# Performance work log

Hardware: AMD Instinct MI355X
Metric: run time of the kernel (lower is better)

The kernel has to match this reference:

```python
import jax, jax.numpy as jnp
import numpy as np

HIDDEN = 128
POOL = 64
G = 4            # grid_size
NBHD = 2.0       # neighborhood_size (meters)
NUM_SCENES = 256
PEDS = 64        # pedestrians per scene (uniform seq_start_end)


def setup_inputs() -> dict:
    key = jax.random.key(0)
    k1, k2, k3 = jax.random.split(key, 3)
    hidden_states = jax.random.normal(k1, (NUM_SCENES * PEDS, HIDDEN), jnp.float32)
    positions = jax.random.uniform(k2, (NUM_SCENES * PEDS, 2), jnp.float32)
    fan_in = HIDDEN * G * G
    weight = jax.random.normal(k3, (fan_in, POOL), jnp.float32) / np.sqrt(fan_in)
    bias = jnp.zeros((POOL,), jnp.float32)
    return {
        "hidden_states": hidden_states,
        "positions": positions,
        "weight": weight,
        "bias": bias,
        "peds_per_scene": PEDS,
    }


def reference(hidden_states, positions, weight, bias, peds_per_scene):
    total, H = hidden_states.shape
    P = peds_per_scene
    B = total // P
    h = hidden_states.reshape(B, P, H)
    p = positions.reshape(B, P, 2)

    # rel[b, i, j] = pos[j] - pos[i]  (matches curr_pos - curr_pos[i:i+1])
    rel = p[:, None, :, :] - p[:, :, None, :]            # [B, P, P, 2]
    in_range = (jnp.abs(rel[..., 0]) <= NBHD) & (jnp.abs(rel[..., 1]) <= NBHD)
    not_self = ~jnp.eye(P, dtype=bool)[None]
    mask = in_range & not_self                            # [B, P, P]

    # int() truncation == floor here since (rel + NBHD) >= 0 inside the range check
    scale = G / (2.0 * NBHD)
    gx = jnp.clip(jnp.floor((rel[..., 0] + NBHD) * scale).astype(jnp.int32), 0, G - 1)
    gy = jnp.clip(jnp.floor((rel[..., 1] + NBHD) * scale).astype(jnp.int32), 0, G - 1)
    grid_idx = gy * G + gx                                # [B, P, P]

    # scatter-add of neighbor hidden states into G*G bins via masked one-hot
    onehot = jax.nn.one_hot(grid_idx, G * G, dtype=h.dtype) * mask[..., None].astype(h.dtype)
    grid = jnp.einsum('bijg,bjh->bigh', onehot, h)        # [B, P, G*G, H]

    flat = grid.reshape(B * P, G * G * H)                 # row-major: (grid_idx, hidden)
    return flat @ weight + bias                            # [total_peds, POOL]
```

## Files before the change

kernel.cpp:

```cpp
#include <hip/hip_runtime.h>
#include <cstdint>

#define PEDS   64
#define HIDDEN 128
#define POOL   64
#define GRIDG  4
#define NBHD   2.0f

typedef unsigned short u16;
typedef unsigned int   u32;
typedef __attribute__((ext_vector_type(8))) short bf16x8;
typedef __attribute__((ext_vector_type(4))) float f32x4;

__device__ __forceinline__ u16 f2bf(float f) {
    u32 u = __float_as_uint(f);
    u += 0x7fffu + ((u >> 16) & 1u);
    return (u16)(u >> 16);
}
__device__ __forceinline__ u32 pack2bf(float a, float b) {
    return (u32)f2bf(a) | ((u32)f2bf(b) << 16);
}

__global__ __launch_bounds__(256, 2) void social_onepass(
    const float* __restrict__ h, const float* __restrict__ pos,
    const float* __restrict__ w, const float* __restrict__ bias,
    float* __restrict__ out)
{
    const int tid  = threadIdx.x;
    const int mt   = tid >> 6;
    const int lane = tid & 63;
    const int l15  = lane & 15;
    const int q    = lane >> 4;
    const int scene = blockIdx.x >> 1;
    const int ch    = blockIdx.x & 1;

    float2 pp = ((const float2*)pos)[(size_t)scene * PEDS + lane];

    const int i = mt * 16 + l15;
    const float pxi = __shfl(pp.x, i), pyi = __shfl(pp.y, i);
    const float scale = (float)GRIDG / (2.0f * NBHD);
    u32 gpk[4] = {0u, 0u, 0u, 0u};
    u32 um = 0u;
#pragma unroll
    for (int kk = 0; kk < 2; ++kk) {
#pragma unroll
        for (int e = 0; e < 8; ++e) {
            int j = kk * 32 + q * 8 + e;
            float rx = __shfl(pp.x, j) - pxi;
            float ry = __shfl(pp.y, j) - pyi;
            u32 gb = 0xffu;
            if ((i != j) && (fabsf(rx) <= NBHD) && (fabsf(ry) <= NBHD)) {
                int gx = (int)floorf((rx + NBHD) * scale); gx = min(max(gx, 0), GRIDG - 1);
                int gy = (int)floorf((ry + NBHD) * scale); gy = min(max(gy, 0), GRIDG - 1);
                gb = (u32)(gy * GRIDG + gx);
                um |= 1u << gb;
            }
            gpk[kk * 2 + (e >> 2)] |= gb << ((e & 3) * 8);
        }
    }
#pragma unroll
    for (int off = 32; off; off >>= 1) um |= __shfl_xor(um, off);
    um = __builtin_amdgcn_readfirstlane(um);

    const float* hbase = h + (size_t)scene * (PEDS * HIDDEN);
    const int jrow = (l15 >> 2) * 8 + (l15 & 3);
    bf16x8 af[16];
#pragma unroll
    for (int mtile = 0; mtile < 4; ++mtile) {
        int jr = (mtile >> 1) * 32 + (mtile & 1) * 4 + jrow;
        const float* rp = hbase + (size_t)jr * HIDDEN + q * 8;
#pragma unroll
        for (int st4 = 0; st4 < 4; ++st4) {
            float4 f0 = *(const float4*)(rp + st4 * 32);
            float4 f1 = *(const float4*)(rp + st4 * 32 + 4);
            union { u32 u[4]; bf16x8 v; } uu;
            uu.u[0] = pack2bf(f0.x, f0.y);
            uu.u[1] = pack2bf(f0.z, f0.w);
            uu.u[2] = pack2bf(f1.x, f1.y);
            uu.u[3] = pack2bf(f1.z, f1.w);
            af[mtile * 4 + st4] = uu.v;
        }
    }

    const float bv0 = bias[ch * 32 + l15];
    const float bv1 = bias[ch * 32 + 16 + l15];
    f32x4 oacc0 = (f32x4){0.f, 0.f, 0.f, 0.f};
    f32x4 oacc1 = (f32x4){0.f, 0.f, 0.f, 0.f};

    const int ng = __popc(um);
    u32 rem = um;
    int g = 0;
    float wf32[64];
    const float* wb = w + ch * 32 + l15;
    if (ng) {
        g = __ffs(rem) - 1; rem &= rem - 1u;
#pragma unroll
        for (int f = 0; f < 8; ++f) {
            int ni = f >> 2, st4 = f & 3;
            const float* src = wb + ((size_t)(g * HIDDEN + st4 * 32 + q * 8)) * POOL + ni * 16;
#pragma unroll
            for (int e = 0; e < 8; ++e) wf32[f * 8 + e] = src[(size_t)e * POOL];
        }
    }

    for (int t = 0; t < ng; ++t) {
        bf16x8 wfrag[8];
#pragma unroll
        for (int f = 0; f < 8; ++f) {
            union { u32 u[4]; bf16x8 v; } uu;
            uu.u[0] = pack2bf(wf32[f * 8 + 0], wf32[f * 8 + 1]);
            uu.u[1] = pack2bf(wf32[f * 8 + 2], wf32[f * 8 + 3]);
            uu.u[2] = pack2bf(wf32[f * 8 + 4], wf32[f * 8 + 5]);
            uu.u[3] = pack2bf(wf32[f * 8 + 6], wf32[f * 8 + 7]);
            wfrag[f] = uu.v;
        }
        const int gcur = g;
        if (rem) {
            g = __ffs(rem) - 1; rem &= rem - 1u;
#pragma unroll
            for (int f = 0; f < 8; ++f) {
                int ni = f >> 2, st4 = f & 3;
                const float* src = wb + ((size_t)(g * HIDDEN + st4 * 32 + q * 8)) * POOL + ni * 16;
#pragma unroll
                for (int e = 0; e < 8; ++e) wf32[f * 8 + e] = src[(size_t)e * POOL];
            }
        }

        f32x4 acc1[4][2];
#pragma unroll
        for (int a = 0; a < 4; ++a) {
            acc1[a][0] = (f32x4){0.f, 0.f, 0.f, 0.f};
            acc1[a][1] = (f32x4){0.f, 0.f, 0.f, 0.f};
        }
#pragma unroll
        for (int st4 = 0; st4 < 4; ++st4) {
#pragma unroll
            for (int mtile = 0; mtile < 4; ++mtile) {
                acc1[mtile][0] = __builtin_amdgcn_mfma_f32_16x16x32_bf16(
                    af[mtile * 4 + st4], wfrag[st4], acc1[mtile][0], 0, 0, 0);
                acc1[mtile][1] = __builtin_amdgcn_mfma_f32_16x16x32_bf16(
                    af[mtile * 4 + st4], wfrag[4 + st4], acc1[mtile][1], 0, 0, 0);
            }
        }

#pragma unroll
        for (int kk = 0; kk < 2; ++kk) {
            u32 wa = gpk[kk * 2], wc = gpk[kk * 2 + 1];
            union { u16 hx[8]; bf16x8 v; } mu;
#pragma unroll
            for (int b = 0; b < 4; ++b)
                mu.hx[b]     = (((wa >> (b * 8)) & 0xffu) == (u32)gcur) ? (u16)0x3F80 : (u16)0;
#pragma unroll
            for (int b = 0; b < 4; ++b)
                mu.hx[4 + b] = (((wc >> (b * 8)) & 0xffu) == (u32)gcur) ? (u16)0x3F80 : (u16)0;
#pragma unroll
            for (int ni = 0; ni < 2; ++ni) {
                union { u32 u[4]; bf16x8 v; } bb;
                bb.u[0] = pack2bf(acc1[kk * 2][ni][0],     acc1[kk * 2][ni][1]);
                bb.u[1] = pack2bf(acc1[kk * 2][ni][2],     acc1[kk * 2][ni][3]);
                bb.u[2] = pack2bf(acc1[kk * 2 + 1][ni][0], acc1[kk * 2 + 1][ni][1]);
                bb.u[3] = pack2bf(acc1[kk * 2 + 1][ni][2], acc1[kk * 2 + 1][ni][3]);
                if (ni == 0)
                    oacc0 = __builtin_amdgcn_mfma_f32_16x16x32_bf16(mu.v, bb.v, oacc0, 0, 0, 0);
                else
                    oacc1 = __builtin_amdgcn_mfma_f32_16x16x32_bf16(mu.v, bb.v, oacc1, 0, 0, 0);
            }
        }
    }

    size_t ob = ((size_t)scene * PEDS + mt * 16 + q * 4) * POOL + ch * 32 + l15;
#pragma unroll
    for (int r = 0; r < 4; ++r) {
        out[ob + (size_t)r * POOL]      = oacc0[r] + bv0;
        out[ob + (size_t)r * POOL + 16] = oacc1[r] + bv1;
    }
}

extern "C" void kernel_launch(void* const* d_in, const int* in_sizes, int n_in,
                              void* d_out, int out_size, void* d_ws, size_t ws_size,
                              hipStream_t stream) {
    const float* h    = (const float*)d_in[0];
    const float* pos  = (const float*)d_in[1];
    const float* w    = (const float*)d_in[2];
    const float* bias = (const float*)d_in[3];
    float* out = (float*)d_out;

    const int total = in_sizes[0] / HIDDEN;
    const int B     = total / PEDS;

    hipLaunchKernelGGL(social_onepass, dim3(B * 2), dim3(256), 0, stream,
                       h, pos, w, bias, out);
}
```

Baseline: 82.74 us.

## Stage bf16 weight tiles in LDS and batch four grid cells per round

Each wave now loads only its own 16 rows of hidden states instead of all 64 rows. The block cooperatively converts weight slices for four occupied grid cells at a time into bf16 in shared memory, and it exchanges h·W partial products through LDS for the masked one-hot MFMA. This drops the redundant per-wave weight loads and the large register arrays, and it raises the occupancy target to 3 blocks. In exchange it adds about 48KB of LDS per block and extra __syncthreads barriers per batch, and unused slots are padded when the cell count is not a multiple of four.

```diff
diff --git a/kernel.cpp b/kernel.cpp
--- a/kernel.cpp
+++ b/kernel.cpp
@@ -21,13 +21,17 @@
     return (u32)f2bf(a) | ((u32)f2bf(b) << 16);
 }
 
-__global__ __launch_bounds__(256, 2) void social_onepass(
+__global__ __launch_bounds__(256, 3) void social_r6(
     const float* __restrict__ h, const float* __restrict__ pos,
     const float* __restrict__ w, const float* __restrict__ bias,
     float* __restrict__ out)
 {
+    __shared__ u16 wtab[16384];
+    __shared__ u16 hwT[8192];
+    __shared__ u32 wmask[4];
+
     const int tid  = threadIdx.x;
-    const int mt   = tid >> 6;
+    const int wv   = tid >> 6;
     const int lane = tid & 63;
     const int l15  = lane & 15;
     const int q    = lane >> 4;
@@ -36,7 +40,7 @@
 
     float2 pp = ((const float2*)pos)[(size_t)scene * PEDS + lane];
 
-    const int i = mt * 16 + l15;
+    const int i = wv * 16 + l15;
     const float pxi = __shfl(pp.x, i), pyi = __shfl(pp.y, i);
     const float scale = (float)GRIDG / (2.0f * NBHD);
     u32 gpk[4] = {0u, 0u, 0u, 0u};
@@ -60,115 +64,117 @@
     }
 #pragma unroll
     for (int off = 32; off; off >>= 1) um |= __shfl_xor(um, off);
-    um = __builtin_amdgcn_readfirstlane(um);
+    if (lane == 0) wmask[wv] = um;
 
-    const float* hbase = h + (size_t)scene * (PEDS * HIDDEN);
-    const int jrow = (l15 >> 2) * 8 + (l15 & 3);
-    bf16x8 af[16];
-#pragma unroll
-    for (int mtile = 0; mtile < 4; ++mtile) {
-        int jr = (mtile >> 1) * 32 + (mtile & 1) * 4 + jrow;
-        const float* rp = hbase + (size_t)jr * HIDDEN + q * 8;
+    bf16x8 af[4];
+    {
+        const float* hr = h + ((size_t)scene * PEDS + wv * 16 + l15) * HIDDEN + q * 8;
 #pragma unroll
         for (int st4 = 0; st4 < 4; ++st4) {
-            float4 f0 = *(const float4*)(rp + st4 * 32);
-            float4 f1 = *(const float4*)(rp + st4 * 32 + 4);
+            float4 f0 = *(const float4*)(hr + st4 * 32);
+            float4 f1 = *(const float4*)(hr + st4 * 32 + 4);
             union { u32 u[4]; bf16x8 v; } uu;
             uu.u[0] = pack2bf(f0.x, f0.y);
             uu.u[1] = pack2bf(f0.z, f0.w);
             uu.u[2] = pack2bf(f1.x, f1.y);
             uu.u[3] = pack2bf(f1.z, f1.w);
-            af[mtile * 4 + st4] = uu.v;
+            af[st4] = uu.v;
         }
     }
-
     const float bv0 = bias[ch * 32 + l15];
     const float bv1 = bias[ch * 32 + 16 + l15];
+
+    __syncthreads();
+    u32 mask = wmask[0] | wmask[1] | wmask[2] | wmask[3];
+    mask = __builtin_amdgcn_readfirstlane(mask);
+
     f32x4 oacc0 = (f32x4){0.f, 0.f, 0.f, 0.f};
     f32x4 oacc1 = (f32x4){0.f, 0.f, 0.f, 0.f};
 
-    const int ng = __popc(um);
-    u32 rem = um;
-    int g = 0;
-    float wf32[64];
-    const float* wb = w + ch * 32 + l15;
-    if (ng) {
-        g = __ffs(rem) - 1; rem &= rem - 1u;
+    const int np = __popc(mask);
+    const int nb = np ? (np + 3) >> 2 : 1;
+    u32 rem = mask;
+
+    const int tl    = tid & 127;
+    const int c4    = tl & 7;
+    const int koct  = tl >> 3;
+    const int slot0 = (tid >> 7) * 2;
+
+    for (int b = 0; b < nb; ++b) {
+        int gs[4];
 #pragma unroll
-        for (int f = 0; f < 8; ++f) {
-            int ni = f >> 2, st4 = f & 3;
-            const float* src = wb + ((size_t)(g * HIDDEN + st4 * 32 + q * 8)) * POOL + ni * 16;
+        for (int t = 0; t < 4; ++t) {
+            gs[t] = rem ? (__ffs(rem) - 1) : -1;
+            if (rem) rem &= rem - 1u;
+        }
+        if (b) __syncthreads();
+
 #pragma unroll
-            for (int e = 0; e < 8; ++e) wf32[f * 8 + e] = src[(size_t)e * POOL];
-        }
-    }
-
-    for (int t = 0; t < ng; ++t) {
-        bf16x8 wfrag[8];
+        for (int tt = 0; tt < 2; ++tt) {
+            int t  = slot0 + tt;
+            int ge = gs[t] < 0 ? 0 : gs[t];
+            const float* src = w + ((size_t)(ge * HIDDEN + koct * 8)) * POOL + ch * 32 + c4 * 4;
+            float4 v[8];
 #pragma unroll
-        for (int f = 0; f < 8; ++f) {
-            union { u32 u[4]; bf16x8 v; } uu;
-            uu.u[0] = pack2bf(wf32[f * 8 + 0], wf32[f * 8 + 1]);
-            uu.u[1] = pack2bf(wf32[f * 8 + 2], wf32[f * 8 + 3]);
-            uu.u[2] = pack2bf(wf32[f * 8 + 4], wf32[f * 8 + 5]);
-            uu.u[3] = pack2bf(wf32[f * 8 + 6], wf32[f * 8 + 7]);
-            wfrag[f] = uu.v;
-        }
-        const int gcur = g;
-        if (rem) {
-            g = __ffs(rem) - 1; rem &= rem - 1u;
+            for (int e = 0; e < 8; ++e) v[e] = *(const float4*)(src + (size_t)e * POOL);
+            const float* vp = (const float*)v;
+            int st4 = koct >> 2, ni = c4 >> 2;
+            int Lb  = (koct & 3) * 16 + (c4 & 3) * 4;
+            uint4* dst = (uint4*)wtab + ((t * 4 + st4) * 2 + ni) * 64 + Lb;
 #pragma unroll
-            for (int f = 0; f < 8; ++f) {
-                int ni = f >> 2, st4 = f & 3;
-                const float* src = wb + ((size_t)(g * HIDDEN + st4 * 32 + q * 8)) * POOL + ni * 16;
-#pragma unroll
-                for (int e = 0; e < 8; ++e) wf32[f * 8 + e] = src[(size_t)e * POOL];
+            for (int ii = 0; ii < 4; ++ii) {
+                dst[ii] = make_uint4(
+                    pack2bf(vp[0 * 4 + ii], vp[1 * 4 + ii]),
+                    pack2bf(vp[2 * 4 + ii], vp[3 * 4 + ii]),
+                    pack2bf(vp[4 * 4 + ii], vp[5 * 4 + ii]),
+                    pack2bf(vp[6 * 4 + ii], vp[7 * 4 + ii]));
             }
         }
+        __syncthreads();
 
-        f32x4 acc1[4][2];
+        const int kkw = wv >> 1;
+        const int c4w = (wv & 1) * 2 + (q >> 1);
+        const int e0  = (q & 1) * 4;
 #pragma unroll
-        for (int a = 0; a < 4; ++a) {
-            acc1[a][0] = (f32x4){0.f, 0.f, 0.f, 0.f};
-            acc1[a][1] = (f32x4){0.f, 0.f, 0.f, 0.f};
+        for (int t = 0; t < 4; ++t) {
+            f32x4 a10 = (f32x4){0.f, 0.f, 0.f, 0.f};
+            f32x4 a11 = (f32x4){0.f, 0.f, 0.f, 0.f};
+#pragma unroll
+            for (int st4 = 0; st4 < 4; ++st4) {
+                bf16x8 b0 = *(const bf16x8*)&wtab[(((t * 4 + st4) * 2 + 0) * 64 + lane) * 8];
+                bf16x8 b1 = *(const bf16x8*)&wtab[(((t * 4 + st4) * 2 + 1) * 64 + lane) * 8];
+                a10 = __builtin_amdgcn_mfma_f32_16x16x32_bf16(af[st4], b0, a10, 0, 0, 0);
+                a11 = __builtin_amdgcn_mfma_f32_16x16x32_bf16(af[st4], b1, a11, 0, 0, 0);
+            }
+            *(uint2*)&hwT[((((t * 2 + kkw) * 4 + c4w) * 2 + 0) * 16 + l15) * 8 + e0] =
+                make_uint2(pack2bf(a10[0], a10[1]), pack2bf(a10[2], a10[3]));
+            *(uint2*)&hwT[((((t * 2 + kkw) * 4 + c4w) * 2 + 1) * 16 + l15) * 8 + e0] =
+                make_uint2(pack2bf(a11[0], a11[1]), pack2bf(a11[2], a11[3]));
         }
-#pragma unroll
-        for (int st4 = 0; st4 < 4; ++st4) {
-#pragma unroll
-            for (int mtile = 0; mtile < 4; ++mtile) {
-                acc1[mtile][0] = __builtin_amdgcn_mfma_f32_16x16x32_bf16(
-                    af[mtile * 4 + st4], wfrag[st4], acc1[mtile][0], 0, 0, 0);
-                acc1[mtile][1] = __builtin_amdgcn_mfma_f32_16x16x32_bf16(
-                    af[mtile * 4 + st4], wfrag[4 + st4], acc1[mtile][1], 0, 0, 0);
-            }
-        }
+        __syncthreads();
 
 #pragma unroll
-        for (int kk = 0; kk < 2; ++kk) {
-            u32 wa = gpk[kk * 2], wc = gpk[kk * 2 + 1];
-            union { u16 hx[8]; bf16x8 v; } mu;
+        for (int t = 0; t < 4; ++t) {
+            u32 gt = (u32)gs[t];
 #pragma unroll
-            for (int b = 0; b < 4; ++b)
-                mu.hx[b]     = (((wa >> (b * 8)) & 0xffu) == (u32)gcur) ? (u16)0x3F80 : (u16)0;
+            for (int kk = 0; kk < 2; ++kk) {
+                u32 wa = gpk[kk * 2], wc = gpk[kk * 2 + 1];
+                union { u16 hx[8]; bf16x8 v; } mu;
 #pragma unroll
-            for (int b = 0; b < 4; ++b)
-                mu.hx[4 + b] = (((wc >> (b * 8)) & 0xffu) == (u32)gcur) ? (u16)0x3F80 : (u16)0;
+                for (int bb_ = 0; bb_ < 4; ++bb_)
+                    mu.hx[bb_]     = (((wa >> (bb_ * 8)) & 0xffu) == gt) ? (u16)0x3F80 : (u16)0;
 #pragma unroll
-            for (int ni = 0; ni < 2; ++ni) {
-                union { u32 u[4]; bf16x8 v; } bb;
-                bb.u[0] = pack2bf(acc1[kk * 2][ni][0],     acc1[kk * 2][ni][1]);
-                bb.u[1] = pack2bf(acc1[kk * 2][ni][2],     acc1[kk * 2][ni][3]);
-                bb.u[2] = pack2bf(acc1[kk * 2 + 1][ni][0], acc1[kk * 2 + 1][ni][1]);
-                bb.u[3] = pack2bf(acc1[kk * 2 + 1][ni][2], acc1[kk * 2 + 1][ni][3]);
-                if (ni == 0)
-                    oacc0 = __builtin_amdgcn_mfma_f32_16x16x32_bf16(mu.v, bb.v, oacc0, 0, 0, 0);
-                else
-                    oacc1 = __builtin_amdgcn_mfma_f32_16x16x32_bf16(mu.v, bb.v, oacc1, 0, 0, 0);
+                for (int bb_ = 0; bb_ < 4; ++bb_)
+                    mu.hx[4 + bb_] = (((wc >> (bb_ * 8)) & 0xffu) == gt) ? (u16)0x3F80 : (u16)0;
+                bf16x8 bb0 = *(const bf16x8*)&hwT[((((t * 2 + kk) * 4 + q) * 2 + 0) * 16 + l15) * 8];
+                bf16x8 bb1 = *(const bf16x8*)&hwT[((((t * 2 + kk) * 4 + q) * 2 + 1) * 16 + l15) * 8];
+                oacc0 = __builtin_amdgcn_mfma_f32_16x16x32_bf16(mu.v, bb0, oacc0, 0, 0, 0);
+                oacc1 = __builtin_amdgcn_mfma_f32_16x16x32_bf16(mu.v, bb1, oacc1, 0, 0, 0);
             }
         }
     }
 
-    size_t ob = ((size_t)scene * PEDS + mt * 16 + q * 4) * POOL + ch * 32 + l15;
+    size_t ob = ((size_t)scene * PEDS + wv * 16 + q * 4) * POOL + ch * 32 + l15;
 #pragma unroll
     for (int r = 0; r < 4; ++r) {
         out[ob + (size_t)r * POOL]      = oacc0[r] + bv0;
@@ -188,6 +194,6 @@
     const int total = in_sizes[0] / HIDDEN;
     const int B     = total / PEDS;
 
-    hipLaunchKernelGGL(social_onepass, dim3(B * 2), dim3(256), 0, stream,
+    hipLaunchKernelGGL(social_r6, dim3(B * 2), dim3(256), 0, stream,
                        h, pos, w, bias, out);
 }
```

After: 72.71 us. 12.1% less time.
